# Performance work log

Hardware: AMD Instinct MI355X
Metric: run time of the kernel (lower is better)

Reference implementation:

```python
import jax, jax.numpy as jnp
import numpy as np

B, S, D, H = 2, 2048, 1024, 16
HD = D // H  # head_dim = 64


def setup_inputs() -> dict:
    key = jax.random.key(0)
    ks = jax.random.split(key, 5)
    scale = 1.0 / np.sqrt(D)
    return {
        "x": jax.random.normal(ks[0], (B, S, D), dtype=jnp.float32),
        "attention_mask": jnp.zeros((B, 1, 1, S), dtype=jnp.float32),
        "Wq": jax.random.normal(ks[1], (D, D), dtype=jnp.float32) * scale,
        "Wk": jax.random.normal(ks[2], (D, D), dtype=jnp.float32) * scale,
        "Wv": jax.random.normal(ks[3], (D, D), dtype=jnp.float32) * scale,
        "Wo": jax.random.normal(ks[4], (D, D), dtype=jnp.float32) * scale,
    }


def reference(x, attention_mask, Wq, Wk, Wv, Wo):
    # nn.Linear applies x @ W.T; weights here stored as [out, in]
    q = jnp.einsum("bsd,ed->bse", x, Wq).reshape(B, S, H, HD).transpose(0, 2, 1, 3)
    k = jnp.einsum("bsd,ed->bse", x, Wk).reshape(B, S, H, HD).transpose(0, 2, 1, 3)
    v = jnp.einsum("bsd,ed->bse", x, Wv).reshape(B, S, H, HD).transpose(0, 2, 1, 3)
    scores = jnp.einsum("bhqd,bhkd->bhqk", q, k) / jnp.sqrt(jnp.float32(HD))
    scores = scores + attention_mask  # additive mask, broadcasts [B,1,1,S]
    attn = jax.nn.softmax(scores, axis=-1)  # dropout p=0 (eval) -> identity
    ctx = jnp.einsum("bhqk,bhkd->bhqd", attn, v)
    ctx = ctx.transpose(0, 2, 1, 3).reshape(B, S, D)
    out = jnp.einsum("bsd,ed->bse", ctx, Wo)
    return out
```

## Files before the change

### kernel.cpp

```cpp
#include <hip/hip_runtime.h>
#include <hip/hip_bf16.h>
#include <cstdint>
#include <cstddef>


#define B_  2
#define S_  2048
#define D_  1024
#define H_  16
#define HD_ 64

typedef __bf16 bf16x8 __attribute__((ext_vector_type(8)));
typedef __bf16 bf16x4 __attribute__((ext_vector_type(4)));
typedef float  f32x4  __attribute__((ext_vector_type(4)));

__device__ __forceinline__ void async16(const __bf16* g, const __bf16* l) {
  __builtin_amdgcn_global_load_lds(
      (const __attribute__((address_space(1))) void*)(uintptr_t)g,
      (__attribute__((address_space(3))) void*)(uint32_t)(uintptr_t)l,
      16, 0, 0);
}

__device__ __forceinline__ unsigned cvt_pk_bf16(float lo, float hi) {
  unsigned r;
  asm("v_cvt_pk_bf16_f32 %0, %1, %2" : "=v"(r) : "v"(lo), "v"(hi));
  return r;
}

__global__ __launch_bounds__(256) void cvt_all(const float* __restrict__ x,
    const float* __restrict__ wq, const float* __restrict__ wk,
    const float* __restrict__ wv, const float* __restrict__ wo,
    __bf16* __restrict__ xb, __bf16* __restrict__ wqb, __bf16* __restrict__ wkb,
    __bf16* __restrict__ wvb, __bf16* __restrict__ wob) {
  const int sel = blockIdx.y;
  const float* src; __bf16* dst; int n;
  if      (sel == 0) { src = x;  dst = xb;  n = B_ * S_ * D_; }
  else if (sel == 1) { src = wq; dst = wqb; n = D_ * D_; }
  else if (sel == 2) { src = wk; dst = wkb; n = D_ * D_; }
  else if (sel == 3) { src = wv; dst = wvb; n = D_ * D_; }
  else               { src = wo; dst = wob; n = D_ * D_; }
  for (int i = blockIdx.x * 256 + threadIdx.x; i * 4 < n; i += gridDim.x * 256) {
    const float4 v = *(const float4*)(src + (size_t)i * 4);
    bf16x4 o;
    o[0] = (__bf16)v.x; o[1] = (__bf16)v.y; o[2] = (__bf16)v.z; o[3] = (__bf16)v.w;
    *(bf16x4*)(dst + (size_t)i * 4) = o;
  }
}

template <typename TC>
__device__ __forceinline__ void gemm97_body(const __bf16* __restrict__ A,
                                            const __bf16* __restrict__ Bm,
                                            TC* __restrict__ C,
                                            const int m0, const int n0,
                                            const int N, const int K) {
  __shared__ __align__(16) __bf16 As[128 * 64];
  __shared__ __align__(16) __bf16 Bs[128 * 64];
  const int tid  = threadIdx.x, lane = tid & 63, wave = tid >> 6;
  const int l15  = lane & 15,   quad = lane >> 4;
  const int wr   = wave >> 1,   wc   = wave & 1;
  const int ebase = wave * 2048 + lane * 8;

  f32x4 acc[4][4] = {};
  for (int k0 = 0; k0 < K; k0 += 64) {
#pragma unroll
    for (int i = 0; i < 4; ++i) {
      const int e = ebase + i * 512;
      const int row = e >> 6, col = e & 63;
      async16(A  + (size_t)(m0 + row) * K + k0 + col, As + (wave * 4 + i) * 512);
      async16(Bm + (size_t)(n0 + row) * K + k0 + col, Bs + (wave * 4 + i) * 512);
    }
    __syncthreads();
#pragma unroll
    for (int kk = 0; kk < 2; ++kk) {
      bf16x8 af[4], bfv[4];
#pragma unroll
      for (int rt = 0; rt < 4; ++rt)
        af[rt] = *(const bf16x8*)(As + (wr * 64 + rt * 16 + l15) * 64 + kk * 32 + quad * 8);
#pragma unroll
      for (int ct = 0; ct < 4; ++ct)
        bfv[ct] = *(const bf16x8*)(Bs + (wc * 64 + ct * 16 + l15) * 64 + kk * 32 + quad * 8);
#pragma unroll
      for (int rt = 0; rt < 4; ++rt)
#pragma unroll
        for (int ct = 0; ct < 4; ++ct)
          acc[rt][ct] = __builtin_amdgcn_mfma_f32_16x16x32_bf16(af[rt], bfv[ct], acc[rt][ct], 0, 0, 0);
    }
    __syncthreads();
  }
#pragma unroll
  for (int rt = 0; rt < 4; ++rt)
#pragma unroll
    for (int ct = 0; ct < 4; ++ct)
#pragma unroll
      for (int r = 0; r < 4; ++r) {
        const int row = m0 + wr * 64 + rt * 16 + quad * 4 + r;
        const int col = n0 + wc * 64 + ct * 16 + l15;
        C[(size_t)row * N + col] = (TC)acc[rt][ct][r];
      }
}

__global__ __launch_bounds__(256) void qkv_gemm(const __bf16* __restrict__ xb,
                                                const __bf16* __restrict__ wq,
                                                const __bf16* __restrict__ wk,
                                                const __bf16* __restrict__ wv,
                                                __bf16* __restrict__ qkv) {
  const int sel = blockIdx.x >> 3;
  const __bf16* Bm = (sel == 0) ? wq : (sel == 1) ? wk : wv;
  __bf16* C = qkv + (size_t)sel * ((size_t)B_ * S_ * D_);
  gemm97_body<__bf16>(xb, Bm, C, blockIdx.y * 128, (blockIdx.x & 7) * 128, D_, D_);
}

__global__ __launch_bounds__(256) void o_gemm(const __bf16* __restrict__ cb,
                                              const __bf16* __restrict__ wo,
                                              float* __restrict__ out) {
  gemm97_body<float>(cb, wo, out, blockIdx.y * 128, blockIdx.x * 128, D_, D_);
}

__global__ __launch_bounds__(256) void vtrans(const __bf16* __restrict__ vb,
                                              __bf16* __restrict__ vt) {
  __shared__ __bf16 tbuf[64][72];
  const int tid = threadIdx.x;
  const int s0 = blockIdx.x * 64, bh = blockIdx.y;
  const int b = bh >> 4, h = bh & 15;
  const __bf16* src = vb + ((size_t)b * S_ + s0) * D_ + h * HD_;
#pragma unroll
  for (int i = 0; i < 2; ++i) {
    const int r = i * 32 + (tid >> 3), c8 = (tid & 7) * 8;
    *(bf16x8*)(&tbuf[r][c8]) = *(const bf16x8*)(src + (size_t)r * D_ + c8);
  }
  __syncthreads();
  __bf16* dst = vt + (size_t)bh * HD_ * S_ + s0;
#pragma unroll
  for (int i = 0; i < 2; ++i) {
    const int hd = i * 32 + (tid >> 3), sc = (tid & 7) * 8;
    bf16x8 v;
#pragma unroll
    for (int j = 0; j < 8; ++j) v[j] = tbuf[sc + j][hd];
    *(bf16x8*)(dst + (size_t)hd * S_ + sc) = v;
  }
}

__global__ __launch_bounds__(512, 4) void attn2(const __bf16* __restrict__ Q,
                                                const __bf16* __restrict__ K,
                                                const __bf16* __restrict__ Vt,
                                                const float* __restrict__ mask,
                                                __bf16* __restrict__ O) {
  constexpr int LKT = 72, LVT = 136;
  __shared__ __align__(16) __bf16 kt[2][128 * LKT];
  __shared__ __align__(16) __bf16 vt[2][64 * LVT];
  __shared__ __align__(16) float  mfull[S_];

  const int tid  = threadIdx.x, lane = tid & 63, wave = tid >> 6;
  const int l15  = lane & 15,   quad = lane >> 4;
  const int b = blockIdx.z, h = blockIdx.y, q0 = blockIdx.x * 128;
  const size_t base   = (size_t)b * S_ * D_ + h * HD_;
  const size_t vtbase = (size_t)(b * H_ + h) * HD_ * S_;
  const int qw = q0 + wave * 16;
  constexpr float LOG2E = 1.44269504088896340736f;
  constexpr float SC    = 0.125f * LOG2E;
  constexpr int  NT     = S_ / 128;

  const int idx0 = tid,        kr0 = idx0 >> 3, kc0 = (idx0 & 7) * 8;
  const int idx1 = 512 + tid,  kr1 = idx1 >> 3, kc1 = (idx1 & 7) * 8;
  const int vr0 = idx0 >> 4, vc0 = (idx0 & 15) * 8;
  const int vr1 = idx1 >> 4, vc1 = (idx1 & 15) * 8;

  bf16x8 qf[2];
#pragma unroll
  for (int kb = 0; kb < 2; ++kb)
    qf[kb] = *(const bf16x8*)(Q + base + (size_t)(qw + l15) * D_ + kb * 32 + quad * 8);

  bf16x8 ones;
#pragma unroll
  for (int j = 0; j < 8; ++j) ones[j] = (__bf16)1.0f;

  float m_run = -1e30f;
  f32x4 oacc[4] = {};
  f32x4 lacc   = {};

  bf16x8 rk0, rk1, rv0, rv1;
  rk0 = *(const bf16x8*)(K + base + (size_t)kr0 * D_ + kc0);
  rk1 = *(const bf16x8*)(K + base + (size_t)kr1 * D_ + kc1);
  rv0 = *(const bf16x8*)(Vt + vtbase + (size_t)vr0 * S_ + vc0);
  rv1 = *(const bf16x8*)(Vt + vtbase + (size_t)vr1 * S_ + vc1);
#pragma unroll
  for (int i = 0; i < S_ / 512; ++i)
    mfull[i * 512 + tid] = mask[(size_t)b * S_ + i * 512 + tid] * LOG2E;
  *(bf16x8*)(&kt[0][kr0 * LKT + kc0]) = rk0;
  *(bf16x8*)(&kt[0][kr1 * LKT + kc1]) = rk1;
  *(bf16x8*)(&vt[0][vr0 * LVT + vc0]) = rv0;
  *(bf16x8*)(&vt[0][vr1 * LVT + vc1]) = rv1;
  __syncthreads();

  for (int t = 0; t < NT; ++t) {
    const int cur = t & 1;
    const int t0  = t * 128;
    const __bf16* ktb = &kt[cur][0];
    const __bf16* vtb = &vt[cur][0];

    if (t + 1 < NT) {
      const int tn = t0 + 128;
      rk0 = *(const bf16x8*)(K + base + (size_t)(tn + kr0) * D_ + kc0);
      rk1 = *(const bf16x8*)(K + base + (size_t)(tn + kr1) * D_ + kc1);
      rv0 = *(const bf16x8*)(Vt + vtbase + (size_t)vr0 * S_ + tn + vc0);
      rv1 = *(const bf16x8*)(Vt + vtbase + (size_t)vr1 * S_ + tn + vc1);
    }

    f32x4 sacc[8] = {};
    __builtin_amdgcn_s_setprio(1);
#pragma unroll
    for (int kti = 0; kti < 8; ++kti) {
      const __bf16* kr = ktb + (kti * 16 + l15) * LKT + quad * 8;
      const bf16x8 a0 = *(const bf16x8*)(kr);
      const bf16x8 a1 = *(const bf16x8*)(kr + 32);
      sacc[kti] = __builtin_amdgcn_mfma_f32_16x16x32_bf16(a0, qf[0], sacc[kti], 0, 0, 0);
      sacc[kti] = __builtin_amdgcn_mfma_f32_16x16x32_bf16(a1, qf[1], sacc[kti], 0, 0, 0);
    }
    __builtin_amdgcn_s_setprio(0);

    f32x4 tm4;
#pragma unroll
    for (int r = 0; r < 4; ++r) tm4[r] = -1e30f;
#pragma unroll
    for (int kti = 0; kti < 8; ++kti) {
      const f32x4 mv = *(const f32x4*)(mfull + t0 + kti * 16 + quad * 4);
#pragma unroll
      for (int r = 0; r < 4; ++r) {
        sacc[kti][r] = sacc[kti][r] * SC + mv[r];
        tm4[r] = fmaxf(tm4[r], sacc[kti][r]);
      }
    }
    float tm = fmaxf(fmaxf(tm4[0], tm4[1]), fmaxf(tm4[2], tm4[3]));
    tm = fmaxf(tm, __shfl_xor(tm, 16));
    tm = fmaxf(tm, __shfl_xor(tm, 32));

    if (!__all(tm <= m_run + 8.f)) {
      const float mnew  = fmaxf(m_run, tm);
      const float alpha = __builtin_amdgcn_exp2f(m_run - mnew);
      m_run = mnew;
#pragma unroll
      for (int r = 0; r < 4; ++r) {
        const float aR = __shfl(alpha, quad * 4 + r);
        lacc[r] *= aR;
#pragma unroll
        for (int nt = 0; nt < 4; ++nt) oacc[nt][r] *= aR;
      }
    }

#pragma unroll
    for (int kb = 0; kb < 4; ++kb) {
      unsigned dd[2][2];
#pragma unroll
      for (int kk = 0; kk < 2; ++kk) {
        const int kti = 2 * kb + kk;
        float p[4];
#pragma unroll
        for (int r = 0; r < 4; ++r)
          p[r] = __builtin_amdgcn_exp2f(sacc[kti][r] - m_run);
        dd[kk][0] = cvt_pk_bf16(p[0], p[1]);
        dd[kk][1] = cvt_pk_bf16(p[2], p[3]);
      }
      unsigned a0 = dd[0][0], b0 = dd[1][0], a1 = dd[0][1], b1 = dd[1][1];
      asm("v_permlane32_swap_b32 %0, %1" : "+v"(a0), "+v"(b0));
      asm("v_permlane16_swap_b32 %0, %1" : "+v"(a0), "+v"(b0));
      asm("v_permlane32_swap_b32 %0, %1" : "+v"(a1), "+v"(b1));
      asm("v_permlane16_swap_b32 %0, %1" : "+v"(a1), "+v"(b1));
      union { unsigned u[4]; bf16x8 v; } pw;
      pw.u[0] = a0; pw.u[1] = a1; pw.u[2] = b0; pw.u[3] = b1;
      const bf16x8 pa = pw.v;
      __builtin_amdgcn_s_setprio(1);
      lacc = __builtin_amdgcn_mfma_f32_16x16x32_bf16(pa, ones, lacc, 0, 0, 0);
#pragma unroll
      for (int nt = 0; nt < 4; ++nt) {
        const bf16x8 vf = *(const bf16x8*)(vtb + (nt * 16 + l15) * LVT + kb * 32 + quad * 8);
        oacc[nt] = __builtin_amdgcn_mfma_f32_16x16x32_bf16(pa, vf, oacc[nt], 0, 0, 0);
      }
      __builtin_amdgcn_s_setprio(0);
    }

    __syncthreads();
    if (t + 1 < NT) {
      const int nxt = cur ^ 1;
      *(bf16x8*)(&kt[nxt][kr0 * LKT + kc0]) = rk0;
      *(bf16x8*)(&kt[nxt][kr1 * LKT + kc1]) = rk1;
      *(bf16x8*)(&vt[nxt][vr0 * LVT + vc0]) = rv0;
      *(bf16x8*)(&vt[nxt][vr1 * LVT + vc1]) = rv1;
    }
    __syncthreads();
  }

#pragma unroll
  for (int r = 0; r < 4; ++r) {
    const float inv = 1.0f / lacc[r];
    const int row = qw + quad * 4 + r;
#pragma unroll
    for (int nt = 0; nt < 4; ++nt)
      O[base + (size_t)row * D_ + nt * 16 + l15] = (__bf16)(oacc[nt][r] * inv);
  }
}

extern "C" void kernel_launch(void* const* d_in, const int* in_sizes, int n_in,
                              void* d_out, int out_size, void* d_ws, size_t ws_size,
                              hipStream_t stream) {
  const float* x    = (const float*)d_in[0];
  const float* mask = (const float*)d_in[1];
  const float* Wq   = (const float*)d_in[2];
  const float* Wk   = (const float*)d_in[3];
  const float* Wv   = (const float*)d_in[4];
  const float* Wo   = (const float*)d_in[5];

  char* ws = (char*)d_ws;
  const size_t MB = 1ull << 20;
  const size_t NT = (size_t)B_ * S_ * D_;
  __bf16* xb  = (__bf16*)(ws);
  __bf16* wqb = (__bf16*)(ws + 8 * MB);
  __bf16* wkb = (__bf16*)(ws + 10 * MB);
  __bf16* wvb = (__bf16*)(ws + 12 * MB);
  __bf16* wob = (__bf16*)(ws + 14 * MB);
  __bf16* qkv = (__bf16*)(ws + 16 * MB);
  __bf16* qb  = qkv;
  __bf16* kb  = qkv + NT;
  __bf16* vb  = qkv + 2 * NT;
  __bf16* vtb = xb;
  __bf16* cb  = vb;

  cvt_all<<<dim3(1024, 5), 256, 0, stream>>>(x, Wq, Wk, Wv, Wo, xb, wqb, wkb, wvb, wob);
  qkv_gemm<<<dim3(24, 32), 256, 0, stream>>>(xb, wqb, wkb, wvb, qkv);
  vtrans<<<dim3(32, 32), 256, 0, stream>>>(vb, vtb);
  attn2<<<dim3(S_ / 128, H_, B_), 512, 0, stream>>>(qb, kb, vtb, mask, cb);
  o_gemm<<<dim3(8, 32), 256, 0, stream>>>(cb, wob, (float*)d_out);
}
```

Before: 219.2 us.

## Fuse V transpose into QKV GEMM epilogue and drop separate vtrans kernel

The QKV GEMM body is inlined so its epilogue can stage results through shared memory. Q and K tiles are written as coalesced 16-byte rows, and V tiles are written already transposed into the layout attention expects. This removes the vtrans launch and its extra read and write of V. The context buffer moves to the xb region so it does not overlap. In exchange, the epilogue gains extra LDS traffic and barriers, the kernel uses more shared memory per block, and the inlined main loop may differ from the original gemm97_body pipelining.

```diff
diff --git a/kernel.cpp b/kernel.cpp
--- a/kernel.cpp
+++ b/kernel.cpp
@@ -104,40 +104,93 @@
                                                 const __bf16* __restrict__ wk,
                                                 const __bf16* __restrict__ wv,
                                                 __bf16* __restrict__ qkv) {
+  __shared__ __align__(16) __bf16 As[128 * 64];
+  __shared__ __align__(16) __bf16 Bs[128 * 64];
+  __shared__ __align__(16) __bf16 cs[64 * 136];
   const int sel = blockIdx.x >> 3;
   const __bf16* Bm = (sel == 0) ? wq : (sel == 1) ? wk : wv;
-  __bf16* C = qkv + (size_t)sel * ((size_t)B_ * S_ * D_);
-  gemm97_body<__bf16>(xb, Bm, C, blockIdx.y * 128, (blockIdx.x & 7) * 128, D_, D_);
+  const int m0 = blockIdx.y * 128, n0 = (blockIdx.x & 7) * 128;
+  constexpr int K = D_, N = D_;
+  constexpr size_t NTE = (size_t)B_ * S_ * D_;
+
+  const int tid  = threadIdx.x, lane = tid & 63, wave = tid >> 6;
+  const int l15  = lane & 15,   quad = lane >> 4;
+  const int wr   = wave >> 1,   wc   = wave & 1;
+  const int ebase = wave * 2048 + lane * 8;
+
+  f32x4 acc[4][4] = {};
+  for (int k0 = 0; k0 < K; k0 += 64) {
+#pragma unroll
+    for (int i = 0; i < 4; ++i) {
+      const int e = ebase + i * 512;
+      const int row = e >> 6, col = e & 63;
+      async16(xb + (size_t)(m0 + row) * K + k0 + col, As + (wave * 4 + i) * 512);
+      async16(Bm + (size_t)(n0 + row) * K + k0 + col, Bs + (wave * 4 + i) * 512);
+    }
+    __syncthreads();
+#pragma unroll
+    for (int kk = 0; kk < 2; ++kk) {
+      bf16x8 af[4], bfv[4];
+#pragma unroll
+      for (int rt = 0; rt < 4; ++rt)
+        af[rt] = *(const bf16x8*)(As + (wr * 64 + rt * 16 + l15) * 64 + kk * 32 + quad * 8);
+#pragma unroll
+      for (int ct = 0; ct < 4; ++ct)
+        bfv[ct] = *(const bf16x8*)(Bs + (wc * 64 + ct * 16 + l15) * 64 + kk * 32 + quad * 8);
+#pragma unroll
+      for (int rt = 0; rt < 4; ++rt)
+#pragma unroll
+        for (int ct = 0; ct < 4; ++ct)
+          acc[rt][ct] = __builtin_amdgcn_mfma_f32_16x16x32_bf16(af[rt], bfv[ct], acc[rt][ct], 0, 0, 0);
+    }
+    __syncthreads();
+  }
+
+  const int b  = m0 >> 11;
+  const int s0 = m0 & (S_ - 1);
+  __bf16* vtb = qkv + 2 * NTE;
+#pragma unroll
+  for (int pass = 0; pass < 2; ++pass) {
+    __syncthreads();
+    if (wr == pass) {
+#pragma unroll
+      for (int rt = 0; rt < 4; ++rt)
+#pragma unroll
+        for (int ct = 0; ct < 4; ++ct)
+#pragma unroll
+          for (int r = 0; r < 4; ++r)
+            cs[(rt * 16 + quad * 4 + r) * 136 + wc * 64 + ct * 16 + l15] =
+                (__bf16)acc[rt][ct][r];
+    }
+    __syncthreads();
+    if (sel < 2) {
+      __bf16* C = qkv + (size_t)sel * NTE;
+      const int cc = tid & 15, rr = tid >> 4;
+#pragma unroll
+      for (int p2 = 0; p2 < 4; ++p2) {
+        const int row = p2 * 16 + rr;
+        const bf16x8 v = *(const bf16x8*)(cs + row * 136 + cc * 8);
+        *(bf16x8*)(C + (size_t)(m0 + pass * 64 + row) * N + n0 + cc * 8) = v;
+      }
+    } else {
+      const int e_loc = tid >> 1, sh = (tid & 1) * 32;
+      __bf16* dst = vtb + (size_t)(b * 1024 + n0 + e_loc) * S_ + s0 + pass * 64 + sh;
+#pragma unroll
+      for (int p2 = 0; p2 < 4; ++p2) {
+        bf16x8 v;
+#pragma unroll
+        for (int j = 0; j < 8; ++j)
+          v[j] = cs[(sh + p2 * 8 + j) * 136 + e_loc];
+        *(bf16x8*)(dst + p2 * 8) = v;
+      }
+    }
+  }
 }
 
 __global__ __launch_bounds__(256) void o_gemm(const __bf16* __restrict__ cb,
                                               const __bf16* __restrict__ wo,
                                               float* __restrict__ out) {
   gemm97_body<float>(cb, wo, out, blockIdx.y * 128, blockIdx.x * 128, D_, D_);
-}
-
-__global__ __launch_bounds__(256) void vtrans(const __bf16* __restrict__ vb,
-                                              __bf16* __restrict__ vt) {
-  __shared__ __bf16 tbuf[64][72];
-  const int tid = threadIdx.x;
-  const int s0 = blockIdx.x * 64, bh = blockIdx.y;
-  const int b = bh >> 4, h = bh & 15;
-  const __bf16* src = vb + ((size_t)b * S_ + s0) * D_ + h * HD_;
-#pragma unroll
-  for (int i = 0; i < 2; ++i) {
-    const int r = i * 32 + (tid >> 3), c8 = (tid & 7) * 8;
-    *(bf16x8*)(&tbuf[r][c8]) = *(const bf16x8*)(src + (size_t)r * D_ + c8);
-  }
-  __syncthreads();
-  __bf16* dst = vt + (size_t)bh * HD_ * S_ + s0;
-#pragma unroll
-  for (int i = 0; i < 2; ++i) {
-    const int hd = i * 32 + (tid >> 3), sc = (tid & 7) * 8;
-    bf16x8 v;
-#pragma unroll
-    for (int j = 0; j < 8; ++j) v[j] = tbuf[sc + j][hd];
-    *(bf16x8*)(dst + (size_t)hd * S_ + sc) = v;
-  }
 }
 
 __global__ __launch_bounds__(512, 4) void attn2(const __bf16* __restrict__ Q,
@@ -320,13 +373,11 @@
   __bf16* qkv = (__bf16*)(ws + 16 * MB);
   __bf16* qb  = qkv;
   __bf16* kb  = qkv + NT;
-  __bf16* vb  = qkv + 2 * NT;
-  __bf16* vtb = xb;
-  __bf16* cb  = vb;
+  __bf16* vtb = qkv + 2 * NT;
+  __bf16* cb  = xb;
 
   cvt_all<<<dim3(1024, 5), 256, 0, stream>>>(x, Wq, Wk, Wv, Wo, xb, wqb, wkb, wvb, wob);
   qkv_gemm<<<dim3(24, 32), 256, 0, stream>>>(xb, wqb, wkb, wvb, qkv);
-  vtrans<<<dim3(32, 32), 256, 0, stream>>>(vb, vtb);
   attn2<<<dim3(S_ / 128, H_, B_), 512, 0, stream>>>(qb, kb, vtb, mask, cb);
   o_gemm<<<dim3(8, 32), 256, 0, stream>>>(cb, wob, (float*)d_out);
 }
```

New measurement: 215.0 us. Within noise of the previous version (-1.9%).
